# Kernel tuning notes

Measured on AMD Instinct MI355X. Metric: run time of the kernel, lower is better.

The kernel has to match this reference:

```python
import jax, jax.numpy as jnp
import numpy as np

B, D, K, NC, F = 2048, 256, 256, 64, 512
EPS = 1e-3           # transport_eps
TAU_MIN = 0.01
TAU_DENOM_MIN = 1e-3


def setup_inputs() -> dict:
    key = jax.random.key(0)
    ks = jax.random.split(key, 8)
    # latents strictly inside the Poincare ball (norm ~0.5 for D=256)
    z = 0.03 * jax.random.normal(ks[0], (B, D), jnp.float32)
    features = jax.random.normal(ks[1], (B, F), jnp.float32)
    # SpectralLinear params (treated as plain linear layers in the reference)
    W_qz = 0.02 * jax.random.normal(ks[2], (K, D), jnp.float32)
    b_qz = jnp.zeros((K,), jnp.float32)
    W_qf = 0.02 * jax.random.normal(ks[3], (K, F), jnp.float32)
    b_qf = jnp.zeros((K,), jnp.float32)
    # full tensorization gamma: [K, D, D]
    q_gamma = 0.02 * jax.random.normal(ks[4], (K, D, D), jnp.float32)
    chart_queries = 0.02 * jax.random.normal(ks[5], (NC, K), jnp.float32)
    return {
        "z": z, "features": features,
        "W_qz": W_qz, "b_qz": b_qz, "W_qf": W_qf, "b_qf": b_qf,
        "q_gamma": q_gamma, "chart_queries": chart_queries,
    }


def reference(z, features, W_qz, b_qz, W_qf, b_qf, q_gamma, chart_queries):
    # centers = chart_queries[:, :latent_dim] (chart_tokens=None path); D == K here
    centers = chart_queries[:, :D]                      # [NC, D]

    # ---- hyperbolic (Poincare ball) distance scores ----
    r2 = jnp.sum(z * z, axis=-1)                        # [B]
    c_sq = jnp.sum(centers * centers, axis=-1)          # [NC]
    diff = z[:, None, :] - centers[None, :, :]          # [B, NC, D]
    dist_sq = jnp.sum(diff * diff, axis=-1)             # [B, NC]
    denom = (1.0 - r2[:, None]) * (1.0 - c_sq[None, :])
    arg = 1.0 + 2.0 * dist_sq / (denom + EPS)
    dist = jnp.arccosh(jnp.maximum(arg, 1.0 + EPS))

    # metric-aware temperature tau(z)
    tau = jnp.maximum(
        jnp.sqrt(jnp.float32(K)) * jnp.maximum(1.0 - r2, TAU_DENOM_MIN) * 0.5,
        TAU_MIN,
    )                                                   # [B]
    scores = -dist / tau[:, None]                       # [B, NC]

    # ---- feature-based refinement (q_feat_proj branch) ----
    q = z @ W_qz.T + b_qz + features @ W_qf.T + b_qf    # [B, K]
    # gamma term: einsum('bij,kij->bk', z outer z, q_gamma) without [B,D,D]
    gz = jnp.einsum('bj,kij->bki', z, q_gamma)          # [B, K, D]
    q = q + jnp.einsum('bki,bi->bk', gz, z)             # [B, K]

    # transported queries: base_queries / lambda(z); (Q/lam) . q == (q @ Q.T)/lam
    r2c = jnp.minimum(r2, 1.0 - EPS)
    lam = 2.0 / (1.0 - r2c + EPS)                       # [B]
    feature_scores = (q @ chart_queries.T) / lam[:, None]  # [B, NC]

    scores = scores + 0.1 * feature_scores / tau[:, None]

    router_weights = jax.nn.softmax(scores, axis=-1)    # [B, NC]
    K_chart = jnp.argmax(router_weights, axis=-1)       # [B]
    return router_weights, K_chart
```

## Files before the change

### kernel.cpp

```cpp
#include <hip/hip_runtime.h>
#include <hip/hip_bf16.h>
#include <hip/hip_fp16.h>


#define B_SZ 2048
#define D_SZ 256
#define K_SZ 256
#define NC_SZ 64
#define F_SZ 512
#define P_SZ 65536

typedef float  floatx4  __attribute__((ext_vector_type(4)));
typedef float  floatx16 __attribute__((ext_vector_type(16)));
typedef _Float16 h8 __attribute__((ext_vector_type(8)));
typedef __fp16  fp16x2 __attribute__((ext_vector_type(2)));
union H8U4 { uint4 u; h8 h; };

#define WS_BEFF  49152
#define WS_CSQ   49216
#define WS_MH    196736
#define WS_WALL  2293888
#define WS_PART  2351232
#define WS_DOT   6938752

__device__ __forceinline__ unsigned pkrtz_u(float a, float b) {
    fp16x2 r = __builtin_amdgcn_cvt_pkrtz(a, b);
    return __builtin_bit_cast(unsigned, r);
}
__device__ __forceinline__ _Float16 h16rtz(float x) {
    fp16x2 r = __builtin_amdgcn_cvt_pkrtz(x, x);
    return (_Float16)r[0];
}
__device__ __forceinline__ unsigned packh2(_Float16 a, _Float16 b) {
    union { _Float16 h[2]; unsigned u; } r; r.h[0] = a; r.h[1] = b; return r.u;
}

__device__ __forceinline__ void gload16(const void* g, void* l) {
    __builtin_amdgcn_global_load_lds(
        (const __attribute__((address_space(1))) unsigned*)g,
        (__attribute__((address_space(3))) unsigned*)l, 16, 0, 0);
}

__global__ __launch_bounds__(256, 4) void mid_kernel(
        const float* __restrict__ gamma, const float* __restrict__ cq,
        const float* __restrict__ Wqz,  const float* __restrict__ bqz,
        const float* __restrict__ Wqf,  const float* __restrict__ bqf,
        float* __restrict__ ws, _Float16* __restrict__ mh) {
    __shared__ __align__(16) float cqL[64*129];
    const int tid = threadIdx.x;
    const int bid = blockIdx.x;

    if (bid < 512) {
        const int w = tid >> 6, lane = tid & 63;
        const int ln = lane & 31, half = lane >> 5;
        const int mt = w >> 1, ns = w & 1;
        const int p0 = bid * 128;
        const int iseg = p0 >> 8, j0 = p0 & 255;
        char* bt = (char*)cqL;

        floatx16 acc0, acc1;
        #pragma unroll
        for (int r = 0; r < 16; ++r) { acc0[r] = 0.f; acc1[r] = 0.f; }

        const float* __restrict__ cqrow = cq + (mt*32 + ln)*256;

        #define STAGE_G(kc, sel)                                              \
            _Pragma("unroll")                                                 \
            for (int e0 = 0; e0 < 2; ++e0) {                                  \
                const int e = e0*256 + tid;                                   \
                gload16(gamma + (size_t)((kc)*16 + (e >> 5))*P_SZ             \
                              + p0 + (e & 31)*4,                              \
                        bt + (sel)*8192 + e*16);                              \
            }

        STAGE_G(0, 0);
        for (int t = 0; t < 16; ++t) {
            __syncthreads();
            if (t < 15) { STAGE_G(t + 1, (t + 1) & 1); }

            const floatx4* ap = (const floatx4*)(cqrow + t*16 + half*8);
            floatx4 ca = ap[0], cb = ap[1];
            H8U4 a;
            a.u.x = pkrtz_u(ca[0], ca[1]); a.u.y = pkrtz_u(ca[2], ca[3]);
            a.u.z = pkrtz_u(cb[0], cb[1]); a.u.w = pkrtz_u(cb[2], cb[3]);

            const char* btc = bt + (t & 1)*8192;
            float g0[8], g1[8];
            #pragma unroll
            for (int kk = 0; kk < 8; ++kk) {
                const int roff = (half*8 + kk)*512;
                g0[kk] = *(const float*)(btc + roff + (ns*64 + ln)*4);
                g1[kk] = *(const float*)(btc + roff + (ns*64 + 32 + ln)*4);
            }
            H8U4 b0, b1;
            b0.u.x = pkrtz_u(g0[0], g0[1]); b0.u.y = pkrtz_u(g0[2], g0[3]);
            b0.u.z = pkrtz_u(g0[4], g0[5]); b0.u.w = pkrtz_u(g0[6], g0[7]);
            b1.u.x = pkrtz_u(g1[0], g1[1]); b1.u.y = pkrtz_u(g1[2], g1[3]);
            b1.u.z = pkrtz_u(g1[4], g1[5]); b1.u.w = pkrtz_u(g1[6], g1[7]);

            acc0 = __builtin_amdgcn_mfma_f32_32x32x16_f16(a.h, b0.h, acc0, 0, 0, 0);
            acc1 = __builtin_amdgcn_mfma_f32_32x32x16_f16(a.h, b1.h, acc1, 0, 0, 0);
        }
        #undef STAGE_G

        #pragma unroll
        for (int r = 0; r < 16; ++r) {
            const int cc = mt*32 + (r&3) + 8*(r>>2) + 4*half;
            const int ja = j0 + ns*64 + ln;
            const int jb = j0 + ns*64 + 32 + ln;
            const size_t base = (size_t)cc*P_SZ + iseg*256;
            mh[base + (((ja >> 3) ^ (cc&31))*8 + (ja & 7))] = (_Float16)acc0[r];
            mh[base + (((jb >> 3) ^ (cc&31))*8 + (jb & 7))] = (_Float16)acc1[r];
        }
        return;
    }

    const int pbid = bid - 512;
    const int w = tid >> 6, c = tid & 63;
    char* wall = (char*)(ws + WS_WALL);

    float a0 = 0.f, a1 = 0.f, a2 = 0.f, a3 = 0.f;
    float bacc = 0.f, cacc = 0.f, cqv = 0.f;
    const int i_or_j = (pbid < 64) ? pbid*4 + w :
                       (pbid < 192) ? (pbid - 64)*4 + w : 0;

    for (int h = 0; h < 2; ++h) {
        #pragma unroll
        for (int s8 = 0; s8 < 8; ++s8) {
            const int e4 = s8*256 + tid;
            const int row = e4 >> 5, col4 = (e4 & 31)*4;
            floatx4 v = *(const floatx4*)(cq + row*256 + h*128 + col4);
            #pragma unroll
            for (int u = 0; u < 4; ++u) cqL[row*129 + col4 + u] = v[u];
        }
        __syncthreads();

        if (pbid < 64) {
            const int i = i_or_j;
            #pragma unroll 8
            for (int kk = 0; kk < 128; kk += 4) {
                const int k = h*128 + kk;
                a0 = fmaf(cqL[c*129 + kk    ], Wqz[(k    )*D_SZ + i], a0);
                a1 = fmaf(cqL[c*129 + kk + 1], Wqz[(k + 1)*D_SZ + i], a1);
                a2 = fmaf(cqL[c*129 + kk + 2], Wqz[(k + 2)*D_SZ + i], a2);
                a3 = fmaf(cqL[c*129 + kk + 3], Wqz[(k + 3)*D_SZ + i], a3);
            }
            if ((i >> 7) == h) cqv = cqL[c*129 + (i & 127)];
        } else if (pbid < 192) {
            const int j = i_or_j;
            #pragma unroll 8
            for (int kk = 0; kk < 128; kk += 4) {
                const int k = h*128 + kk;
                a0 = fmaf(cqL[c*129 + kk    ], Wqf[(k    )*F_SZ + j], a0);
                a1 = fmaf(cqL[c*129 + kk + 1], Wqf[(k + 1)*F_SZ + j], a1);
                a2 = fmaf(cqL[c*129 + kk + 2], Wqf[(k + 2)*F_SZ + j], a2);
                a3 = fmaf(cqL[c*129 + kk + 3], Wqf[(k + 3)*F_SZ + j], a3);
            }
        } else {
            if (w == 0) {
                for (int kk = 0; kk < 128; ++kk) {
                    const int k = h*128 + kk;
                    bacc = fmaf(cqL[c*129 + kk], bqz[k] + bqf[k], bacc);
                }
            } else if (w == 1) {
                for (int ii = 0; ii < 128; ++ii) {
                    const float v = cqL[c*129 + ii];
                    cacc = fmaf(v, v, cacc);
                }
            }
        }
        __syncthreads();
    }

    if (pbid < 64) {
        const int i = i_or_j;
        const int boff = c*512 + ((((i >> 3) & 31) ^ (c & 31)) << 4) + (i & 7)*2;
        *(_Float16*)(wall + 0*32768 + boff) = (_Float16)((a0 + a1) + (a2 + a3));
        const _Float16 vh = (_Float16)cqv;
        *(_Float16*)(wall + 5*32768 + boff) = vh;
        *(_Float16*)(wall + 6*32768 + boff) = h16rtz((cqv - (float)vh) * 1024.f);
    } else if (pbid < 192) {
        const int j = i_or_j;
        const float acc = (a0 + a1) + (a2 + a3);
        const int row = j & 255;
        const int sbase = (j < 256) ? 1 : 3;
        const int boff = c*512 + ((((row >> 3) & 31) ^ (c & 31)) << 4) + (row & 7)*2;
        const _Float16 ah = (_Float16)acc;
        *(_Float16*)(wall + (size_t)sbase*32768 + boff) = ah;
        *(_Float16*)(wall + (size_t)(sbase + 1)*32768 + boff) =
            h16rtz((acc - (float)ah) * 1024.f);
    } else {
        if (w == 0) ws[WS_BEFF + c] = bacc;
        else if (w == 1) ws[WS_CSQ + c] = cacc;
    }
}

__global__ __launch_bounds__(256, 3) void qflin_kernel(
        const float* __restrict__ z, const float* __restrict__ feat,
        const _Float16* __restrict__ mh, const float* __restrict__ wall_f,
        float* __restrict__ part, float* __restrict__ dot) {
    __shared__ __align__(16) char bt[2][16384];
    const int tid = threadIdx.x;
    const int w = tid >> 6, lane = tid & 63;
    const int ln = lane & 31, half = lane >> 5;

    if (blockIdx.x >= 64) {
        const int bid = blockIdx.x - 64;
        const int xcd = bid & 7;
        const int y   = bid >> 3;
        const int ig  = xcd*4 + (y & 3);
        const int b0  = (y >> 2) * 128;
        const int bb  = b0 + w*32 + ln;

        #define STAGE_Q(ii, hs, sel)                                          \
            _Pragma("unroll")                                                 \
            for (int e0 = 0; e0 < 4; ++e0) {                                  \
                const int e = e0*256 + tid;                                   \
                const int cc = e >> 4, up = e & 15;                           \
                const int u = (((hs) ^ ((cc >> 4) & 1)) << 4) | up;           \
                gload16((const char*)mh +                                     \
                        ((size_t)cc*P_SZ + (size_t)(ii)*256)*2 + u*16,        \
                        bt[sel] + e*16);                                      \
            }

        STAGE_Q(ig*8, 0, 0);

        uint4 zjh[16];
        #pragma unroll
        for (int ch = 0; ch < 16; ++ch) {
            const floatx4* zp = (const floatx4*)(z + bb*D_SZ + ch*16 + half*8);
            floatx4 a = zp[0], b = zp[1];
            zjh[ch].x = pkrtz_u(a[0], a[1]);
            zjh[ch].y = pkrtz_u(a[2], a[3]);
            zjh[ch].z = pkrtz_u(b[0], b[1]);
            zjh[ch].w = pkrtz_u(b[2], b[3]);
        }
        float ziv[8];
        {
            const floatx4* zp = (const floatx4*)(z + bb*D_SZ + ig*8);
            floatx4 a = zp[0], b = zp[1];
            #pragma unroll
            for (int t = 0; t < 4; ++t) { ziv[t] = a[t]; ziv[4+t] = b[t]; }
        }

        floatx16 acc0, acc1;
        #pragma unroll
        for (int r = 0; r < 16; ++r) { acc0[r] = 0.f; acc1[r] = 0.f; }

        for (int t = 0; t < 16; ++t) {
            __syncthreads();
            if (t < 15) {
                const int tn = t + 1;
                STAGE_Q(ig*8 + (tn >> 1), tn & 1, tn & 1);
            }
            const int il = t >> 1, hs = t & 1;
            const float zi = ziv[il];
            const unsigned zu = pkrtz_u(zi, zi);
            H8U4 zb; zb.u.x = zu; zb.u.y = zu; zb.u.z = zu; zb.u.w = zu;
            const char* btc = bt[t & 1];
            __builtin_amdgcn_s_setprio(1);
            #pragma unroll
            for (int chp = 0; chp < 8; ++chp) {
                H8U4 aj; aj.u = zjh[hs*8 + chp];
                h8 af = aj.h * zb.h;
                const int po = (((chp*2 + half) ^ (ln & 15)) << 4);
                H8U4 f0, f1;
                f0.u = *(const uint4*)(btc + ln*256 + po);
                f1.u = *(const uint4*)(btc + 8192 + ln*256 + po);
                acc0 = __builtin_amdgcn_mfma_f32_32x32x16_f16(af, f0.h, acc0, 0, 0, 0);
                acc1 = __builtin_amdgcn_mfma_f32_32x32x16_f16(af, f1.h, acc1, 0, 0, 0);
            }
            __builtin_amdgcn_s_setprio(0);
        }
        #undef STAGE_Q

        float* __restrict__ qp = part + (size_t)ig * (B_SZ * NC_SZ);
        #pragma unroll
        for (int r = 0; r < 16; ++r) {
            const int row  = (r&3) + 8*(r>>2) + 4*half;
            const int brow = b0 + w*32 + row;
            qp[brow*NC_SZ + ln]      = acc0[r];
            qp[brow*NC_SZ + 32 + ln] = acc1[r];
        }
        return;
    }

    const char* wall = (const char*)wall_f;
    const int lbid = blockIdx.x;
    const int b0 = (lbid >> 2) * 128;
    const int s  = lbid & 3;
    const int bb = b0 + w*32 + ln;
    const int s_hi = (s == 0) ? 0 : (s == 1) ? 1 : (s == 2) ? 3 : 5;
    const float* __restrict__ arow =
        (s == 0 || s == 3) ? z + bb*D_SZ : feat + bb*F_SZ + (s == 2 ? 256 : 0);

    #define STAGE_L(img, h, sel)                                              \
        _Pragma("unroll")                                                     \
        for (int e0 = 0; e0 < 4; ++e0) {                                      \
            const int e = e0*256 + tid;                                       \
            const int cc = e >> 4, up = e & 15;                               \
            const int u = (((h) ^ ((cc >> 4) & 1)) << 4) | up;                \
            gload16(wall + (size_t)(img)*32768 + cc*512 + u*16,               \
                    bt[sel] + e*16);                                          \
        }

    floatx16 hh0, hh1, lh0, lh1, hl0, hl1;
    #pragma unroll
    for (int r = 0; r < 16; ++r) {
        hh0[r] = 0.f; hh1[r] = 0.f; lh0[r] = 0.f;
        lh1[r] = 0.f; hl0[r] = 0.f; hl1[r] = 0.f;
    }

    for (int h = 0; h < 2; ++h) {
        STAGE_L(s_hi, h, 0);
        if (s > 0) { STAGE_L(s_hi + 1, h, 1); }
        __syncthreads();

        #pragma unroll
        for (int chp = 0; chp < 8; ++chp) {
            const int kb = h*128 + chp*16 + half*8;
            const floatx4* ap = (const floatx4*)(arow + kb);
            floatx4 a4 = ap[0], b4 = ap[1];
            float vv[8];
            #pragma unroll
            for (int t = 0; t < 4; ++t) { vv[t] = a4[t]; vv[4+t] = b4[t]; }
            _Float16 hc[8];
            #pragma unroll
            for (int j = 0; j < 8; ++j) hc[j] = (_Float16)vv[j];
            H8U4 ah;
            ah.u.x = packh2(hc[0], hc[1]); ah.u.y = packh2(hc[2], hc[3]);
            ah.u.z = packh2(hc[4], hc[5]); ah.u.w = packh2(hc[6], hc[7]);

            const int po = (((chp*2 + half) ^ (ln & 15)) << 4);
            H8U4 f0, f1;
            f0.u = *(const uint4*)(bt[0] + ln*256 + po);
            f1.u = *(const uint4*)(bt[0] + 8192 + ln*256 + po);
            hh0 = __builtin_amdgcn_mfma_f32_32x32x16_f16(ah.h, f0.h, hh0, 0, 0, 0);
            hh1 = __builtin_amdgcn_mfma_f32_32x32x16_f16(ah.h, f1.h, hh1, 0, 0, 0);

            if (s > 0) {
                float l[8];
                #pragma unroll
                for (int j = 0; j < 8; ++j) l[j] = (vv[j] - (float)hc[j]) * 1024.f;
                H8U4 al;
                al.u.x = pkrtz_u(l[0], l[1]); al.u.y = pkrtz_u(l[2], l[3]);
                al.u.z = pkrtz_u(l[4], l[5]); al.u.w = pkrtz_u(l[6], l[7]);
                H8U4 g0, g1;
                g0.u = *(const uint4*)(bt[1] + ln*256 + po);
                g1.u = *(const uint4*)(bt[1] + 8192 + ln*256 + po);
                lh0 = __builtin_amdgcn_mfma_f32_32x32x16_f16(al.h, f0.h, lh0, 0, 0, 0);
                lh1 = __builtin_amdgcn_mfma_f32_32x32x16_f16(al.h, f1.h, lh1, 0, 0, 0);
                hl0 = __builtin_amdgcn_mfma_f32_32x32x16_f16(ah.h, g0.h, hl0, 0, 0, 0);
                hl1 = __builtin_amdgcn_mfma_f32_32x32x16_f16(ah.h, g1.h, hl1, 0, 0, 0);
            }
        }
        if (h == 0) __syncthreads();
    }
    #undef STAGE_L

    const float is = 1.0f / 1024.0f;
    float* __restrict__ qp = part + (size_t)(32 + s) * (B_SZ * NC_SZ);
    #pragma unroll
    for (int r = 0; r < 16; ++r) {
        const int row  = (r&3) + 8*(r>>2) + 4*half;
        const int brow = b0 + w*32 + row;
        float v0 = hh0[r], v1 = hh1[r];
        if (s > 0) { v0 += (lh0[r] + hl0[r])*is; v1 += (lh1[r] + hl1[r])*is; }
        if (s < 3) {
            qp[brow*NC_SZ + ln]      = v0;
            qp[brow*NC_SZ + 32 + ln] = v1;
        } else {
            dot[brow*NC_SZ + ln]      = v0;
            dot[brow*NC_SZ + 32 + ln] = v1;
        }
    }
}

__global__ __launch_bounds__(256) void final_kernel(
        const float* __restrict__ z, const float* __restrict__ ws,
        const float* __restrict__ dot, float* __restrict__ out) {
    const int w = threadIdx.x >> 6, c = threadIdx.x & 63;
    const int b = blockIdx.x*4 + w;

    const floatx4 zv = *(const floatx4*)(z + b*D_SZ + c*4);
    float r2 = zv[0]*zv[0] + zv[1]*zv[1] + zv[2]*zv[2] + zv[3]*zv[3];
    #pragma unroll
    for (int off = 32; off > 0; off >>= 1)
        r2 += __shfl_xor(r2, off, 64);

    const float* __restrict__ part = ws + WS_PART;
    float Q = ws[WS_BEFF + c];
    #pragma unroll
    for (int p = 0; p < 35; ++p)
        Q += part[(size_t)p * (B_SZ*NC_SZ) + b*NC_SZ + c];

    const float csq = ws[WS_CSQ + c];
    const float dsq = fmaf(-2.f, dot[b*64 + c], r2) + csq;

    const double r2d = (double)r2, csqd = (double)csq, dsqd = (double)dsq;
    const double denom = (1.0 - r2d) * (1.0 - csqd);
    double arg = 1.0 + 2.0 * dsqd / (denom + 0.001);
    if (arg < 1.001) arg = 1.001;
    const double dist = acosh(arg);
    double tmp = 1.0 - r2d; if (tmp < 0.001) tmp = 0.001;
    double tau = 8.0 * tmp;
    if (tau < 0.01) tau = 0.01;
    double r2c = r2d; if (r2c > 0.999) r2c = 0.999;
    const double lam = 2.0 / (1.0 - r2c + 0.001);
    const double score = -dist / tau + 0.1 * ((double)Q / lam) / tau;

    double m = score;
    #pragma unroll
    for (int off = 32; off > 0; off >>= 1) {
        double o = __shfl_xor(m, off, 64);
        m = fmax(m, o);
    }
    const double e = exp(score - m);
    double s = e;
    #pragma unroll
    for (int off = 32; off > 0; off >>= 1) s += __shfl_xor(s, off, 64);
    out[b*NC_SZ + c] = (float)(e / s);

    double bsc = score; int bix = c;
    #pragma unroll
    for (int off = 32; off > 0; off >>= 1) {
        double osc = __shfl_xor(bsc, off, 64);
        int    oix = __shfl_xor(bix, off, 64);
        if (osc > bsc || (osc == bsc && oix < bix)) { bsc = osc; bix = oix; }
    }
    if (c == 0) out[B_SZ*NC_SZ + b] = (float)bix;
}

extern "C" void kernel_launch(void* const* d_in, const int* in_sizes, int n_in,
                              void* d_out, int out_size, void* d_ws, size_t ws_size,
                              hipStream_t stream) {
    const float* z    = (const float*)d_in[0];
    const float* feat = (const float*)d_in[1];
    const float* Wqz  = (const float*)d_in[2];
    const float* bqz  = (const float*)d_in[3];
    const float* Wqf  = (const float*)d_in[4];
    const float* bqf  = (const float*)d_in[5];
    const float* gamma= (const float*)d_in[6];
    const float* cq   = (const float*)d_in[7];
    float* out = (float*)d_out;
    float* ws  = (float*)d_ws;
    _Float16* mh = (_Float16*)(ws + WS_MH);

    mid_kernel<<<705, 256, 0, stream>>>(gamma, cq, Wqz, bqz, Wqf, bqf, ws, mh);
    qflin_kernel<<<576, 256, 0, stream>>>(z, feat, mh, ws + WS_WALL,
                                          ws + WS_PART, ws + WS_DOT);
    final_kernel<<<512, 256, 0, stream>>>(z, ws, ws + WS_DOT, out);
}
```

Baseline: 152.3 us.

## Triple-buffer gamma staging with explicit vmcnt waits and preloaded A fragments

The gamma-contraction phase of mid_kernel moves from a double-buffered loop with a full __syncthreads per step to a fully unrolled three-stage pipeline. It keeps two asynchronous global-to-LDS loads in flight and waits with partial s_waitcnt vmcnt counts before a raw s_barrier. The chart-query A fragments are loaded and converted to fp16 once up front into 16 registers instead of inside every step. Launch bounds drop from 4 to 3 waves per SIMD to leave room for the extra registers, trading occupancy for deeper latency hiding. The third 8 KB buffer fits inside the existing cqL shared array.

```diff
diff --git a/kernel.cpp b/kernel.cpp
--- a/kernel.cpp
+++ b/kernel.cpp
@@ -41,7 +41,7 @@
         (__attribute__((address_space(3))) unsigned*)l, 16, 0, 0);
 }
 
-__global__ __launch_bounds__(256, 4) void mid_kernel(
+__global__ __launch_bounds__(256, 3) void mid_kernel(
         const float* __restrict__ gamma, const float* __restrict__ cq,
         const float* __restrict__ Wqz,  const float* __restrict__ bqz,
         const float* __restrict__ Wqf,  const float* __restrict__ bqf,
@@ -58,11 +58,19 @@
         const int iseg = p0 >> 8, j0 = p0 & 255;
         char* bt = (char*)cqL;
 
+        const float* __restrict__ cqrow = cq + (mt*32 + ln)*256;
+        uint4 af[16];
+        #pragma unroll
+        for (int t = 0; t < 16; ++t) {
+            const floatx4* ap = (const floatx4*)(cqrow + t*16 + half*8);
+            floatx4 ca = ap[0], cb = ap[1];
+            af[t].x = pkrtz_u(ca[0], ca[1]); af[t].y = pkrtz_u(ca[2], ca[3]);
+            af[t].z = pkrtz_u(cb[0], cb[1]); af[t].w = pkrtz_u(cb[2], cb[3]);
+        }
+
         floatx16 acc0, acc1;
         #pragma unroll
         for (int r = 0; r < 16; ++r) { acc0[r] = 0.f; acc1[r] = 0.f; }
-
-        const float* __restrict__ cqrow = cq + (mt*32 + ln)*256;
 
         #define STAGE_G(kc, sel)                                              \
             _Pragma("unroll")                                                 \
@@ -74,33 +82,36 @@
             }
 
         STAGE_G(0, 0);
-        for (int t = 0; t < 16; ++t) {
-            __syncthreads();
-            if (t < 15) { STAGE_G(t + 1, (t + 1) & 1); }
-
-            const floatx4* ap = (const floatx4*)(cqrow + t*16 + half*8);
-            floatx4 ca = ap[0], cb = ap[1];
-            H8U4 a;
-            a.u.x = pkrtz_u(ca[0], ca[1]); a.u.y = pkrtz_u(ca[2], ca[3]);
-            a.u.z = pkrtz_u(cb[0], cb[1]); a.u.w = pkrtz_u(cb[2], cb[3]);
-
-            const char* btc = bt + (t & 1)*8192;
-            float g0[8], g1[8];
-            #pragma unroll
-            for (int kk = 0; kk < 8; ++kk) {
-                const int roff = (half*8 + kk)*512;
-                g0[kk] = *(const float*)(btc + roff + (ns*64 + ln)*4);
-                g1[kk] = *(const float*)(btc + roff + (ns*64 + 32 + ln)*4);
-            }
-            H8U4 b0, b1;
-            b0.u.x = pkrtz_u(g0[0], g0[1]); b0.u.y = pkrtz_u(g0[2], g0[3]);
-            b0.u.z = pkrtz_u(g0[4], g0[5]); b0.u.w = pkrtz_u(g0[6], g0[7]);
-            b1.u.x = pkrtz_u(g1[0], g1[1]); b1.u.y = pkrtz_u(g1[2], g1[3]);
-            b1.u.z = pkrtz_u(g1[4], g1[5]); b1.u.w = pkrtz_u(g1[6], g1[7]);
-
-            acc0 = __builtin_amdgcn_mfma_f32_32x32x16_f16(a.h, b0.h, acc0, 0, 0, 0);
-            acc1 = __builtin_amdgcn_mfma_f32_32x32x16_f16(a.h, b1.h, acc1, 0, 0, 0);
-        }
+        STAGE_G(1, 1);
+
+        #define MC_STEP(T, VMN)                                               \
+        {                                                                     \
+            asm volatile("s_waitcnt vmcnt(" #VMN ")" ::: "memory");           \
+            __builtin_amdgcn_s_barrier();                                     \
+            if ((T) < 14) { STAGE_G((T) + 2, ((T) + 2) % 3); }                \
+            const char* btc = bt + ((T) % 3)*8192;                            \
+            float g0[8], g1[8];                                               \
+            _Pragma("unroll")                                                 \
+            for (int kk = 0; kk < 8; ++kk) {                                  \
+                const int roff = (half*8 + kk)*512;                           \
+                g0[kk] = *(const float*)(btc + roff + (ns*64 + ln)*4);        \
+                g1[kk] = *(const float*)(btc + roff + (ns*64 + 32 + ln)*4);   \
+            }                                                                 \
+            H8U4 a; a.u = af[T];                                              \
+            H8U4 b0, b1;                                                      \
+            b0.u.x = pkrtz_u(g0[0], g0[1]); b0.u.y = pkrtz_u(g0[2], g0[3]);   \
+            b0.u.z = pkrtz_u(g0[4], g0[5]); b0.u.w = pkrtz_u(g0[6], g0[7]);   \
+            b1.u.x = pkrtz_u(g1[0], g1[1]); b1.u.y = pkrtz_u(g1[2], g1[3]);   \
+            b1.u.z = pkrtz_u(g1[4], g1[5]); b1.u.w = pkrtz_u(g1[6], g1[7]);   \
+            acc0 = __builtin_amdgcn_mfma_f32_32x32x16_f16(a.h, b0.h, acc0, 0, 0, 0); \
+            acc1 = __builtin_amdgcn_mfma_f32_32x32x16_f16(a.h, b1.h, acc1, 0, 0, 0); \
+        }
+
+        MC_STEP(0, 2);  MC_STEP(1, 2);  MC_STEP(2, 2);  MC_STEP(3, 2);
+        MC_STEP(4, 2);  MC_STEP(5, 2);  MC_STEP(6, 2);  MC_STEP(7, 2);
+        MC_STEP(8, 2);  MC_STEP(9, 2);  MC_STEP(10, 2); MC_STEP(11, 2);
+        MC_STEP(12, 2); MC_STEP(13, 2); MC_STEP(14, 2); MC_STEP(15, 0);
+        #undef MC_STEP
         #undef STAGE_G
 
         #pragma unroll
```

After: 156.5 us. 2.8% more time.
